# Kernel tuning notes

Measured on AMD Instinct MI355X. Metric: run time of the kernel, lower is better.

## Reference

```python
import jax, jax.numpy as jnp
import numpy as np

B, N, C, H = 4, 8192, 1024, 16
D = C // H

def setup_inputs() -> dict:
    key = jax.random.key(0)
    k1, k2, k3 = jax.random.split(key, 3)
    scale_in = 1.0 / np.sqrt(C)
    return {
        "x": jax.random.normal(k1, (B, N, C), dtype=jnp.float32),
        "w_qkv": jax.random.normal(k2, (C, 3 * C), dtype=jnp.float32) * scale_in,
        "b_qkv": jnp.zeros((3 * C,), dtype=jnp.float32),
        "w_proj": jax.random.normal(k3, (C, C), dtype=jnp.float32) * scale_in,
        "b_proj": jnp.zeros((C,), dtype=jnp.float32),
    }

def reference(x, w_qkv, b_qkv, w_proj, b_proj):
    Bx, Nx, Cx = x.shape
    qkv = x @ w_qkv + b_qkv                       # [B,N,3C]
    qkv = qkv.reshape(Bx, Nx, 3, H, D)
    qkv = jnp.transpose(qkv, (2, 0, 3, 1, 4))     # [3,B,H,N,D]
    q, k, v = qkv[0], qkv[1], qkv[2]
    q = jax.nn.elu(q) + 1.0                       # positive feature map
    k = jax.nn.elu(k) + 1.0
    kv = jnp.einsum('bhnd,bhne->bhde', k, v)      # [B,H,D,D]
    out = jnp.einsum('bhnd,bhde->bhne', q, kv)    # [B,H,N,D]
    z = 1.0 / (jnp.einsum('bhnd,bhd->bhn', q, k.sum(axis=2)) + 1e-8)
    out = out * z[..., None]
    out = jnp.transpose(out, (0, 2, 1, 3)).reshape(Bx, Nx, Cx)
    out = out @ w_proj + b_proj                   # dropout is identity in eval
    return out
```

## Files before the change

### kernel.cpp

```cpp
#include <hip/hip_runtime.h>
#include <hip/hip_bf16.h>
#include <stdint.h>

typedef unsigned short ushort_t;
typedef __attribute__((ext_vector_type(8))) short short8;
typedef __attribute__((ext_vector_type(4))) float floatx4;

__device__ __forceinline__ ushort_t f2b(float f) {
    unsigned u = __float_as_uint(f);
    unsigned r = (u + 0x7FFFu + ((u >> 16) & 1u)) >> 16;
    return (ushort_t)r;
}
__device__ __forceinline__ float b2f(ushort_t h) {
    return __uint_as_float(((unsigned)h) << 16);
}
__device__ __forceinline__ float elu1(float f) {
    return (f > 0.f) ? (f + 1.f) : __expf(f);
}

#define GLDS16(srcp, dstp)                                                          \
    __builtin_amdgcn_global_load_lds(                                               \
        (const __attribute__((address_space(1))) unsigned int*)(srcp),              \
        (__attribute__((address_space(3))) unsigned int*)(dstp), 16, 0, 0)


__global__ void conv_bf16(const float* __restrict__ in, ushort_t* __restrict__ out, int n8) {
    for (int i = blockIdx.x * blockDim.x + threadIdx.x; i < n8; i += gridDim.x * blockDim.x) {
        const float4 f0 = *(const float4*)&in[(size_t)i * 8];
        const float4 f1 = *(const float4*)&in[(size_t)i * 8 + 4];
        ushort4 o0, o1;
        o0.x = f2b(f0.x); o0.y = f2b(f0.y); o0.z = f2b(f0.z); o0.w = f2b(f0.w);
        o1.x = f2b(f1.x); o1.y = f2b(f1.y); o1.z = f2b(f1.z); o1.w = f2b(f1.w);
        *(ushort4*)&out[(size_t)i * 8]     = o0;
        *(ushort4*)&out[(size_t)i * 8 + 4] = o1;
    }
}

__global__ void transpose_conv(const float* __restrict__ in, ushort_t* __restrict__ out,
                               int R, int C) {
    __shared__ float tile[32][33];
    int c0 = blockIdx.x * 32, r0 = blockIdx.y * 32;
    int tx = threadIdx.x, ty = threadIdx.y;
#pragma unroll
    for (int k = 0; k < 4; ++k) {
        int a = ty * 4 + k;
        tile[a][tx] = in[(size_t)(r0 + a) * C + c0 + tx];
    }
    __syncthreads();
#pragma unroll
    for (int k = 0; k < 4; ++k) {
        int a = ty * 4 + k;
        out[(size_t)(c0 + a) * R + r0 + tx] = f2b(tile[tx][a]);
    }
}

__global__ void zero_f32(float* __restrict__ p, int n) {
    int i = blockIdx.x * blockDim.x + threadIdx.x;
    if (i < n) p[i] = 0.f;
}

template<int MODE>
__global__ __launch_bounds__(512, 2) void gemm256(
    const ushort_t* __restrict__ A, const ushort_t* __restrict__ Bt,
    const float* __restrict__ bias,
    ushort_t* __restrict__ out_u16, float* __restrict__ out_f32,
    int Nt, int nbx)
{
    extern __shared__ ushort_t lds[];
    constexpr int KK = 1024;

    const int tid  = threadIdx.x;
    const int wave = tid >> 6;
    const int lane = tid & 63;
    const int wm_i = wave >> 2;
    const int wn_i = wave & 3;
    const int fr   = lane & 15;
    const int fq   = lane >> 4;

    const int nwg = (int)gridDim.x;
    const int bid = (int)blockIdx.x;
    const int swz = (bid & 7) * (nwg >> 3) + (bid >> 3);
    const int bx = swz % nbx, by = swz / nbx;
    const int m0 = by * 256, n0 = bx * 256;

    const int trow = tid >> 3;
    const int csw  = ((tid & 7) ^ (trow & 7)) << 3;
    const int tcolB = ((tid >> 8) << 6) + (trow & 31);

    const ushort_t* sa = A  + (size_t)(m0 + trow)  * KK + csw;
    const ushort_t* sb = Bt + (size_t)(n0 + tcolB) * KK + csw;

    const int dstA = wave * 512;
    const int dstB = 16384 + wave * 512;

    const int sw0 = (fq ^ (fr & 7)) << 3;
    const int sw1 = sw0 ^ 32;
    const int abase = (wm_i * 64 + fr) * 64;
    const int bbase = (wn_i * 32 + fr) * 64;
    int loA0[2][2], loA1[2][2], loB0[2][2], loB1[2][2];
#pragma unroll
    for (int bf = 0; bf < 2; ++bf)
#pragma unroll
        for (int q = 0; q < 2; ++q) {
            loA0[bf][q] = bf * 32768 + q * 8192 + abase + sw0;
            loA1[bf][q] = bf * 32768 + q * 8192 + abase + sw1;
            loB0[bf][q] = bf * 32768 + 16384 + q * 8192 + bbase + sw0;
            loB1[bf][q] = bf * 32768 + 16384 + q * 8192 + bbase + sw1;
        }

    floatx4 acc[8][4];
    const floatx4 z4 = {0.f, 0.f, 0.f, 0.f};
#pragma unroll
    for (int i = 0; i < 8; ++i)
#pragma unroll
        for (int j = 0; j < 4; ++j) acc[i][j] = z4;

    short8 a[4][2], b[2][2];

    auto stageA = [&](int buf, int h, int ko) {
        ushort_t* d = lds + buf * 32768 + h * 8192 + dstA;
        GLDS16(sa + h * (64 * KK) + ko, d);
        GLDS16(sa + h * (64 * KK) + 128 * KK + ko, d + 4096);
    };
    auto stageB = [&](int buf, int h, int ko) {
        ushort_t* d = lds + buf * 32768 + h * 8192 + dstB;
        GLDS16(sb + h * (32 * KK) + ko, d);
        GLDS16(sb + h * (32 * KK) + 128 * KK + ko, d + 4096);
    };
    auto loadA = [&](int buf, int qr) {
        const int o0 = loA0[buf][qr], o1 = loA1[buf][qr];
#pragma unroll
        for (int i = 0; i < 4; ++i) {
            a[i][0] = *(const short8*)(lds + o0 + i * 1024);
            a[i][1] = *(const short8*)(lds + o1 + i * 1024);
        }
    };
    auto loadB = [&](int buf, int qc) {
        const int o0 = loB0[buf][qc], o1 = loB1[buf][qc];
#pragma unroll
        for (int j = 0; j < 2; ++j) {
            b[j][0] = *(const short8*)(lds + o0 + j * 1024);
            b[j][1] = *(const short8*)(lds + o1 + j * 1024);
        }
    };
    auto mma = [&](int qr, int qc) {
#pragma unroll
        for (int i = 0; i < 4; ++i)
#pragma unroll
            for (int j = 0; j < 2; ++j) {
                acc[qr * 4 + i][qc * 2 + j] =
                    __builtin_amdgcn_mfma_f32_16x16x32_bf16(b[j][0], a[i][0], acc[qr * 4 + i][qc * 2 + j], 0, 0, 0);
                acc[qr * 4 + i][qc * 2 + j] =
                    __builtin_amdgcn_mfma_f32_16x16x32_bf16(b[j][1], a[i][1], acc[qr * 4 + i][qc * 2 + j], 0, 0, 0);
            }
    };

#define PRIO1() __builtin_amdgcn_s_setprio(1)
#define BOUT()  __builtin_amdgcn_s_setprio(0); __builtin_amdgcn_s_barrier()
#define VM6()   asm volatile("s_waitcnt vmcnt(6)" ::: "memory")
#define VM0()   asm volatile("s_waitcnt vmcnt(0)" ::: "memory")

    stageA(0, 0, 0);
    stageB(0, 1, 0);
    stageA(0, 1, 0);
    stageB(0, 0, 0);
    stageA(1, 0, 64);
    stageB(1, 1, 64);
    stageA(1, 1, 64);
    VM6();
    __builtin_amdgcn_s_barrier();

    int ko = 0;
    for (int pr = 0; pr < 7; ++pr, ko += 128) {
        loadA(0, 0); loadB(0, 0);
        stageB(1, 0, ko + 64);
        PRIO1(); mma(0, 0); BOUT();

        loadB(0, 1);
        stageA(0, 0, ko + 128);
        PRIO1(); mma(0, 1); BOUT();

        loadA(0, 1);
        stageB(0, 1, ko + 128);
        PRIO1(); mma(1, 1); BOUT();

        loadB(0, 0);
        stageA(0, 1, ko + 128);
        PRIO1(); mma(1, 0); __builtin_amdgcn_s_setprio(0); VM6();
        __builtin_amdgcn_s_barrier();

        loadA(1, 0); loadB(1, 0);
        stageB(0, 0, ko + 128);
        PRIO1(); mma(0, 0); BOUT();

        loadB(1, 1);
        stageA(1, 0, ko + 192);
        PRIO1(); mma(0, 1); BOUT();

        loadA(1, 1);
        stageB(1, 1, ko + 192);
        PRIO1(); mma(1, 1); BOUT();

        loadB(1, 0);
        stageA(1, 1, ko + 192);
        PRIO1(); mma(1, 0); __builtin_amdgcn_s_setprio(0); VM6();
        __builtin_amdgcn_s_barrier();
    }

    loadA(0, 0); loadB(0, 0);
    stageB(1, 0, 960);
    PRIO1(); mma(0, 0); BOUT();

    loadB(0, 1);
    PRIO1(); mma(0, 1); BOUT();

    loadA(0, 1);
    PRIO1(); mma(1, 1); BOUT();

    loadB(0, 0);
    PRIO1(); mma(1, 0); __builtin_amdgcn_s_setprio(0); VM0();
    __builtin_amdgcn_s_barrier();

    loadA(1, 0); loadB(1, 0);
    PRIO1(); mma(0, 0); BOUT();

    loadB(1, 1);
    PRIO1(); mma(0, 1); BOUT();

    loadA(1, 1);
    PRIO1(); mma(1, 1); BOUT();

    loadB(1, 0);
    PRIO1(); mma(1, 0);
    __builtin_amdgcn_s_setprio(0);

#undef PRIO1
#undef BOUT
#undef VM6
#undef VM0

    float4 bv[4];
#pragma unroll
    for (int cj = 0; cj < 4; ++cj) {
        const int nb = n0 + wn_i * 64 + (cj >> 1) * 32 + (cj & 1) * 16 + fq * 4;
        bv[cj] = *(const float4*)&bias[nb];
    }
#pragma unroll
    for (int ri = 0; ri < 8; ++ri) {
        const int m = m0 + wm_i * 128 + (ri >> 2) * 64 + (ri & 3) * 16 + fr;
#pragma unroll
        for (int cj = 0; cj < 4; ++cj) {
            const int col = n0 + wn_i * 64 + (cj >> 1) * 32 + (cj & 1) * 16 + fq * 4;
            if (MODE == 0) {
                const int s = col >> 10;
                const int c = col & 1023;
                const int h = c >> 6;
                const int d = c & 63;
                const int bb = m >> 13;
                const int n  = m & 8191;
                float v0 = acc[ri][cj][0] + bv[cj].x;
                float v1 = acc[ri][cj][1] + bv[cj].y;
                float v2 = acc[ri][cj][2] + bv[cj].z;
                float v3 = acc[ri][cj][3] + bv[cj].w;
                if (s < 2) { v0 = elu1(v0); v1 = elu1(v1); v2 = elu1(v2); v3 = elu1(v3); }
                ushort4 o;
                o.x = f2b(v0); o.y = f2b(v1); o.z = f2b(v2); o.w = f2b(v3);
                *(ushort4*)&out_u16[(((size_t)s * 64 + bb * 16 + h) * 8192 + n) * 64 + d] = o;
            } else {
                float4 o;
                o.x = acc[ri][cj][0] + bv[cj].x;
                o.y = acc[ri][cj][1] + bv[cj].y;
                o.z = acc[ri][cj][2] + bv[cj].z;
                o.w = acc[ri][cj][3] + bv[cj].w;
                *(float4*)&out_f32[(size_t)m * Nt + col] = o;
            }
        }
    }
}

__global__ __launch_bounds__(256) void kv_kernel(
    const ushort_t* __restrict__ kbuf, const ushort_t* __restrict__ vbuf,
    float* __restrict__ kv, float* __restrict__ ksum)
{
    __shared__ ushort_t ks[64 * 64] __attribute__((aligned(16)));
    __shared__ ushort_t vs[64 * 64] __attribute__((aligned(16)));

    const int bh = blockIdx.y, chunk = blockIdx.x, t = threadIdx.x;
    const int d0 = (t >> 4) * 4, e0 = (t & 15) * 4;
    const bool do_ksum = (t & 15) == 0;

    float acc[4][4];
#pragma unroll
    for (int i = 0; i < 4; ++i)
#pragma unroll
        for (int j = 0; j < 4; ++j) acc[i][j] = 0.f;
    float kacc[4] = {0.f, 0.f, 0.f, 0.f};

    for (int sub = 0; sub < 8; ++sub) {
        const int nb = chunk * 512 + sub * 64;
        __syncthreads();
#pragma unroll
        for (int p = 0; p < 2; ++p) {
            int idx = p * 256 + t;
            int r = idx >> 3, c = (idx & 7) * 8;
            *(short8*)&ks[r * 64 + c] = *(const short8*)&kbuf[((size_t)bh * 8192 + nb + r) * 64 + c];
            *(short8*)&vs[r * 64 + c] = *(const short8*)&vbuf[((size_t)bh * 8192 + nb + r) * 64 + c];
        }
        __syncthreads();
        for (int n = 0; n < 64; ++n) {
            ushort4 kd = *(const ushort4*)&ks[n * 64 + d0];
            ushort4 ve = *(const ushort4*)&vs[n * 64 + e0];
            float kf[4] = {b2f(kd.x), b2f(kd.y), b2f(kd.z), b2f(kd.w)};
            float vf[4] = {b2f(ve.x), b2f(ve.y), b2f(ve.z), b2f(ve.w)};
#pragma unroll
            for (int i = 0; i < 4; ++i) {
#pragma unroll
                for (int j = 0; j < 4; ++j) acc[i][j] += kf[i] * vf[j];
            }
            if (do_ksum) {
#pragma unroll
                for (int i = 0; i < 4; ++i) kacc[i] += kf[i];
            }
        }
    }
#pragma unroll
    for (int i = 0; i < 4; ++i) {
        if (do_ksum) atomicAdd(&ksum[bh * 64 + d0 + i], kacc[i]);
#pragma unroll
        for (int j = 0; j < 4; ++j)
            atomicAdd(&kv[((size_t)bh * 64 + d0 + i) * 64 + e0 + j], acc[i][j]);
    }
}

__global__ __launch_bounds__(256) void out_kernel(
    const ushort_t* __restrict__ qbuf, const float* __restrict__ kv,
    const float* __restrict__ ksum, ushort_t* __restrict__ obuf)
{
    __shared__ float kvs[4096];
    __shared__ float ksums[64];

    const int bh = blockIdx.y, chunk = blockIdx.x, t = threadIdx.x;
    const int b = bh >> 4, h = bh & 15;
    const int wave = t >> 6, lane = t & 63;
    const int tok = lane & 15, fq = lane >> 4;

#pragma unroll
    for (int i = 0; i < 4; ++i) {
        int idx = (i * 256 + t) * 4;
        *(float4*)&kvs[idx] = *(const float4*)&kv[(size_t)bh * 4096 + idx];
    }
    if (t < 64) ksums[t] = ksum[bh * 64 + t];
    __syncthreads();

    short8 afr[4][2];
#pragma unroll
    for (int et = 0; et < 4; ++et)
#pragma unroll
        for (int kslice = 0; kslice < 2; ++kslice)
#pragma unroll
            for (int i = 0; i < 8; ++i) {
                const int d = kslice * 32 + fq * 8 + i;
                afr[et][kslice][i] = (short)f2b(kvs[d * 64 + et * 16 + tok]);
            }
    short8 zfr[2];
#pragma unroll
    for (int kslice = 0; kslice < 2; ++kslice)
#pragma unroll
        for (int i = 0; i < 8; ++i)
            zfr[kslice][i] = (short)f2b(ksums[kslice * 32 + fq * 8 + i]);

    const floatx4 z4 = {0.f, 0.f, 0.f, 0.f};
    const int nbase = chunk * 1024 + wave * 256;
    const ushort_t* qrow = qbuf + ((size_t)bh * 8192 + nbase + tok) * 64 + fq * 8;
    ushort_t* orow = obuf + ((size_t)b * 8192 + nbase + tok) * 1024 + h * 64 + fq * 4;

#pragma unroll 2
    for (int g = 0; g < 16; ++g) {
        short8 bf0 = *(const short8*)(qrow + (size_t)g * 16 * 64);
        short8 bf1 = *(const short8*)(qrow + (size_t)g * 16 * 64 + 32);

        floatx4 az = __builtin_amdgcn_mfma_f32_16x16x32_bf16(zfr[0], bf0, z4, 0, 0, 0);
        az = __builtin_amdgcn_mfma_f32_16x16x32_bf16(zfr[1], bf1, az, 0, 0, 0);

        floatx4 ad[4];
#pragma unroll
        for (int et = 0; et < 4; ++et) {
            ad[et] = __builtin_amdgcn_mfma_f32_16x16x32_bf16(afr[et][0], bf0, z4, 0, 0, 0);
            ad[et] = __builtin_amdgcn_mfma_f32_16x16x32_bf16(afr[et][1], bf1, ad[et], 0, 0, 0);
        }

        const float zi = 1.f / (az[0] + 1e-8f);
#pragma unroll
        for (int et = 0; et < 4; ++et) {
            ushort4 o;
            o.x = f2b(ad[et][0] * zi);
            o.y = f2b(ad[et][1] * zi);
            o.z = f2b(ad[et][2] * zi);
            o.w = f2b(ad[et][3] * zi);
            *(ushort4*)&orow[(size_t)g * 16 * 1024 + et * 16] = o;
        }
    }
}


extern "C" void kernel_launch(void* const* d_in, const int* in_sizes, int n_in,
                              void* d_out, int out_size, void* d_ws, size_t ws_size,
                              hipStream_t stream) {
    const float* x      = (const float*)d_in[0];
    const float* w_qkv  = (const float*)d_in[1];
    const float* b_qkv  = (const float*)d_in[2];
    const float* w_proj = (const float*)d_in[3];
    const float* b_proj = (const float*)d_in[4];
    float* out = (float*)d_out;

    const size_t XE = (size_t)32768 * 1024;

    char* ws = (char*)d_ws;
    ushort_t* xb   = (ushort_t*)ws;  ws += XE * 2;
    ushort_t* wqT  = (ushort_t*)ws;  ws += (size_t)3072 * 1024 * 2;
    ushort_t* wpT  = (ushort_t*)ws;  ws += (size_t)1024 * 1024 * 2;
    ushort_t* qkvb = (ushort_t*)ws;  ws += 3 * XE * 2;
    ushort_t* ob   = (ushort_t*)ws;  ws += XE * 2;
    float*    kv   = (float*)ws;     ws += (size_t)64 * 64 * 64 * 4;
    float*    ksum = (float*)ws;     ws += (size_t)64 * 64 * 4;

    (void)hipFuncSetAttribute(reinterpret_cast<const void*>(gemm256<0>),
                              hipFuncAttributeMaxDynamicSharedMemorySize, 131072);
    (void)hipFuncSetAttribute(reinterpret_cast<const void*>(gemm256<1>),
                              hipFuncAttributeMaxDynamicSharedMemorySize, 131072);

    zero_f32<<<dim3((64 * 64 * 64 + 64 * 64 + 255) / 256), dim3(256), 0, stream>>>(kv, 64 * 64 * 64 + 64 * 64);
    conv_bf16<<<dim3(2048), dim3(256), 0, stream>>>(x, xb, (int)(XE / 8));
    transpose_conv<<<dim3(96, 32), dim3(32, 8), 0, stream>>>(w_qkv, wqT, 1024, 3072);
    transpose_conv<<<dim3(32, 32), dim3(32, 8), 0, stream>>>(w_proj, wpT, 1024, 1024);

    gemm256<0><<<dim3(1536), dim3(512), 131072, stream>>>(xb, wqT, b_qkv, qkvb, nullptr, 3072, 12);

    kv_kernel<<<dim3(16, 64), dim3(256), 0, stream>>>(qkvb + XE, qkvb + 2 * XE, kv, ksum);
    out_kernel<<<dim3(8, 64), dim3(256), 0, stream>>>(qkvb, kv, ksum, ob);

    gemm256<1><<<dim3(512), dim3(512), 131072, stream>>>(ob, wpT, b_proj, nullptr, out, 1024, 4);
}
```

Baseline: 490.3 us.

## Switch GEMM inner product to 32x32x16 bf16 MFMA tiles

Replaces the 16x16x32 MFMA fragments in the 256x256 GEMM with 32x32x16 MFMA instructions. This changes the LDS read fragment layout, the accumulator shape (floatx16), and the epilogue index mapping. The larger MFMA issues fewer instructions and gets more reuse per LDS read, at the cost of a different swizzle access pattern that may cause LDS bank conflicts. The epilogue also uses the hardware packed bf16 convert instruction instead of manual rounding.

```diff
diff --git a/kernel.cpp b/kernel.cpp
--- a/kernel.cpp
+++ b/kernel.cpp
@@ -5,6 +5,7 @@
 typedef unsigned short ushort_t;
 typedef __attribute__((ext_vector_type(8))) short short8;
 typedef __attribute__((ext_vector_type(4))) float floatx4;
+typedef __attribute__((ext_vector_type(16))) float floatx16;
 
 __device__ __forceinline__ ushort_t f2b(float f) {
     unsigned u = __float_as_uint(f);
@@ -16,6 +17,11 @@
 }
 __device__ __forceinline__ float elu1(float f) {
     return (f > 0.f) ? (f + 1.f) : __expf(f);
+}
+__device__ __forceinline__ unsigned cvtpk(float lo, float hi) {
+    unsigned w;
+    asm("v_cvt_pk_bf16_f32 %0, %1, %2" : "=v"(w) : "v"(lo), "v"(hi));
+    return w;
 }
 
 #define GLDS16(srcp, dstp)                                                          \
@@ -74,8 +80,8 @@
     const int lane = tid & 63;
     const int wm_i = wave >> 2;
     const int wn_i = wave & 3;
-    const int fr   = lane & 15;
-    const int fq   = lane >> 4;
+    const int ml   = lane & 31;
+    const int fh   = lane >> 5;
 
     const int nwg = (int)gridDim.x;
     const int bid = (int)blockIdx.x;
@@ -93,29 +99,21 @@
     const int dstA = wave * 512;
     const int dstB = 16384 + wave * 512;
 
-    const int sw0 = (fq ^ (fr & 7)) << 3;
-    const int sw1 = sw0 ^ 32;
-    const int abase = (wm_i * 64 + fr) * 64;
-    const int bbase = (wn_i * 32 + fr) * 64;
-    int loA0[2][2], loA1[2][2], loB0[2][2], loB1[2][2];
-#pragma unroll
-    for (int bf = 0; bf < 2; ++bf)
-#pragma unroll
-        for (int q = 0; q < 2; ++q) {
-            loA0[bf][q] = bf * 32768 + q * 8192 + abase + sw0;
-            loA1[bf][q] = bf * 32768 + q * 8192 + abase + sw1;
-            loB0[bf][q] = bf * 32768 + 16384 + q * 8192 + bbase + sw0;
-            loB1[bf][q] = bf * 32768 + 16384 + q * 8192 + bbase + sw1;
-        }
-
-    floatx4 acc[8][4];
-    const floatx4 z4 = {0.f, 0.f, 0.f, 0.f};
-#pragma unroll
-    for (int i = 0; i < 8; ++i)
-#pragma unroll
-        for (int j = 0; j < 4; ++j) acc[i][j] = z4;
-
-    short8 a[4][2], b[2][2];
+    int pcs[4];
+#pragma unroll
+    for (int s = 0; s < 4; ++s) pcs[s] = (((s * 2 + fh) ^ (lane & 7)) << 3);
+    const int rbA = (wm_i * 64 + ml) << 6;
+    const int rbB = (wn_i * 32 + ml) << 6;
+
+    floatx16 acc[4][2];
+#pragma unroll
+    for (int i = 0; i < 4; ++i)
+#pragma unroll
+        for (int j = 0; j < 2; ++j)
+#pragma unroll
+            for (int e = 0; e < 16; ++e) acc[i][j][e] = 0.f;
+
+    short8 a32[2][4], b32[4];
 
     auto stageA = [&](int buf, int h, int ko) {
         ushort_t* d = lds + buf * 32768 + h * 8192 + dstA;
@@ -128,31 +126,27 @@
         GLDS16(sb + h * (32 * KK) + 128 * KK + ko, d + 4096);
     };
     auto loadA = [&](int buf, int qr) {
-        const int o0 = loA0[buf][qr], o1 = loA1[buf][qr];
-#pragma unroll
-        for (int i = 0; i < 4; ++i) {
-            a[i][0] = *(const short8*)(lds + o0 + i * 1024);
-            a[i][1] = *(const short8*)(lds + o1 + i * 1024);
-        }
+        const int base = buf * 32768 + qr * 8192 + rbA;
+#pragma unroll
+        for (int i = 0; i < 2; ++i)
+#pragma unroll
+            for (int s = 0; s < 4; ++s)
+                a32[i][s] = *(const short8*)(lds + base + i * 2048 + pcs[s]);
     };
     auto loadB = [&](int buf, int qc) {
-        const int o0 = loB0[buf][qc], o1 = loB1[buf][qc];
-#pragma unroll
-        for (int j = 0; j < 2; ++j) {
-            b[j][0] = *(const short8*)(lds + o0 + j * 1024);
-            b[j][1] = *(const short8*)(lds + o1 + j * 1024);
-        }
+        const int base = buf * 32768 + 16384 + qc * 8192 + rbB;
+#pragma unroll
+        for (int s = 0; s < 4; ++s)
+            b32[s] = *(const short8*)(lds + base + pcs[s]);
     };
     auto mma = [&](int qr, int qc) {
 #pragma unroll
-        for (int i = 0; i < 4; ++i)
-#pragma unroll
-            for (int j = 0; j < 2; ++j) {
-                acc[qr * 4 + i][qc * 2 + j] =
-                    __builtin_amdgcn_mfma_f32_16x16x32_bf16(b[j][0], a[i][0], acc[qr * 4 + i][qc * 2 + j], 0, 0, 0);
-                acc[qr * 4 + i][qc * 2 + j] =
-                    __builtin_amdgcn_mfma_f32_16x16x32_bf16(b[j][1], a[i][1], acc[qr * 4 + i][qc * 2 + j], 0, 0, 0);
-            }
+        for (int s = 0; s < 4; ++s) {
+            acc[qr * 2 + 0][qc] =
+                __builtin_amdgcn_mfma_f32_32x32x16_bf16(b32[s], a32[0][s], acc[qr * 2 + 0][qc], 0, 0, 0);
+            acc[qr * 2 + 1][qc] =
+                __builtin_amdgcn_mfma_f32_32x32x16_bf16(b32[s], a32[1][s], acc[qr * 2 + 1][qc], 0, 0, 0);
+        }
     };
 
 #define PRIO1() __builtin_amdgcn_s_setprio(1)
@@ -239,40 +233,42 @@
 #undef VM6
 #undef VM0
 
-    float4 bv[4];
-#pragma unroll
-    for (int cj = 0; cj < 4; ++cj) {
-        const int nb = n0 + wn_i * 64 + (cj >> 1) * 32 + (cj & 1) * 16 + fq * 4;
-        bv[cj] = *(const float4*)&bias[nb];
-    }
-#pragma unroll
-    for (int ri = 0; ri < 8; ++ri) {
-        const int m = m0 + wm_i * 128 + (ri >> 2) * 64 + (ri & 3) * 16 + fr;
-#pragma unroll
-        for (int cj = 0; cj < 4; ++cj) {
-            const int col = n0 + wn_i * 64 + (cj >> 1) * 32 + (cj & 1) * 16 + fq * 4;
-            if (MODE == 0) {
-                const int s = col >> 10;
-                const int c = col & 1023;
-                const int h = c >> 6;
-                const int d = c & 63;
-                const int bb = m >> 13;
-                const int n  = m & 8191;
-                float v0 = acc[ri][cj][0] + bv[cj].x;
-                float v1 = acc[ri][cj][1] + bv[cj].y;
-                float v2 = acc[ri][cj][2] + bv[cj].z;
-                float v3 = acc[ri][cj][3] + bv[cj].w;
-                if (s < 2) { v0 = elu1(v0); v1 = elu1(v1); v2 = elu1(v2); v3 = elu1(v3); }
-                ushort4 o;
-                o.x = f2b(v0); o.y = f2b(v1); o.z = f2b(v2); o.w = f2b(v3);
-                *(ushort4*)&out_u16[(((size_t)s * 64 + bb * 16 + h) * 8192 + n) * 64 + d] = o;
-            } else {
-                float4 o;
-                o.x = acc[ri][cj][0] + bv[cj].x;
-                o.y = acc[ri][cj][1] + bv[cj].y;
-                o.z = acc[ri][cj][2] + bv[cj].z;
-                o.w = acc[ri][cj][3] + bv[cj].w;
-                *(float4*)&out_f32[(size_t)m * Nt + col] = o;
+    float4 bvv[2][4];
+#pragma unroll
+    for (int qch = 0; qch < 2; ++qch)
+#pragma unroll
+        for (int g = 0; g < 4; ++g) {
+            const int nb = n0 + wn_i * 64 + qch * 32 + 8 * g + 4 * fh;
+            bvv[qch][g] = *(const float4*)&bias[nb];
+        }
+#pragma unroll
+    for (int mt = 0; mt < 4; ++mt) {
+        const int m = m0 + wm_i * 128 + mt * 32 + ml;
+#pragma unroll
+        for (int qch = 0; qch < 2; ++qch) {
+#pragma unroll
+            for (int g = 0; g < 4; ++g) {
+                const int nb = n0 + wn_i * 64 + qch * 32 + 8 * g + 4 * fh;
+                float v0 = acc[mt][qch][4 * g + 0] + bvv[qch][g].x;
+                float v1 = acc[mt][qch][4 * g + 1] + bvv[qch][g].y;
+                float v2 = acc[mt][qch][4 * g + 2] + bvv[qch][g].z;
+                float v3 = acc[mt][qch][4 * g + 3] + bvv[qch][g].w;
+                if (MODE == 0) {
+                    const int s  = nb >> 10;
+                    const int c  = nb & 1023;
+                    const int hh = c >> 6;
+                    const int d  = c & 63;
+                    const int bb = m >> 13;
+                    const int nt = m & 8191;
+                    if (s < 2) { v0 = elu1(v0); v1 = elu1(v1); v2 = elu1(v2); v3 = elu1(v3); }
+                    uint2 o;
+                    o.x = cvtpk(v0, v1);
+                    o.y = cvtpk(v2, v3);
+                    *(uint2*)&out_u16[(((size_t)s * 64 + bb * 16 + hh) * 8192 + nt) * 64 + d] = o;
+                } else {
+                    float4 o; o.x = v0; o.y = v1; o.z = v2; o.w = v3;
+                    *(float4*)&out_f32[(size_t)m * Nt + nb] = o;
+                }
             }
         }
     }
```

Result: slower. 534.8 us (+9.1%).

## Compute K^T V with MFMA using transposed K/V layout from QKV GEMM epilogue

Applied to the files above, without the earlier changes.

The QKV GEMM epilogue now writes K and V transposed (d-major, token-contiguous), so a new kernel can load token strips per head-dim row and run bf16 MFMA to form K^T V, with ksum obtained by an MFMA against a ones vector. Per-wave partials are reduced in LDS before the atomics, and the grid uses fewer, larger chunks. This replaces the scalar FMA outer-product loop, which was ALU bound. The cost is that the epilogue's K/V writes become scattered 2-byte stores with a large stride instead of vectorized ushort4 stores, which may slow the GEMM.

```diff
diff --git a/kernel.cpp b/kernel.cpp
--- a/kernel.cpp
+++ b/kernel.cpp
@@ -68,6 +68,7 @@
 {
     extern __shared__ ushort_t lds[];
     constexpr int KK = 1024;
+    constexpr size_t XEc = (size_t)32768 * 1024;
 
     const int tid  = threadIdx.x;
     const int wave = tid >> 6;
@@ -251,84 +252,146 @@
 #pragma unroll
         for (int cj = 0; cj < 4; ++cj) {
             const int col = n0 + wn_i * 64 + (cj >> 1) * 32 + (cj & 1) * 16 + fq * 4;
+            float v0 = acc[ri][cj][0] + bv[cj].x;
+            float v1 = acc[ri][cj][1] + bv[cj].y;
+            float v2 = acc[ri][cj][2] + bv[cj].z;
+            float v3 = acc[ri][cj][3] + bv[cj].w;
             if (MODE == 0) {
-                const int s = col >> 10;
-                const int c = col & 1023;
-                const int h = c >> 6;
-                const int d = c & 63;
+                const int s  = col >> 10;
+                const int c  = col & 1023;
+                const int h  = c >> 6;
+                const int d  = c & 63;
                 const int bb = m >> 13;
                 const int n  = m & 8191;
-                float v0 = acc[ri][cj][0] + bv[cj].x;
-                float v1 = acc[ri][cj][1] + bv[cj].y;
-                float v2 = acc[ri][cj][2] + bv[cj].z;
-                float v3 = acc[ri][cj][3] + bv[cj].w;
-                if (s < 2) { v0 = elu1(v0); v1 = elu1(v1); v2 = elu1(v2); v3 = elu1(v3); }
-                ushort4 o;
-                o.x = f2b(v0); o.y = f2b(v1); o.z = f2b(v2); o.w = f2b(v3);
-                *(ushort4*)&out_u16[(((size_t)s * 64 + bb * 16 + h) * 8192 + n) * 64 + d] = o;
+                const int bh = bb * 16 + h;
+                if (s == 0) {
+                    v0 = elu1(v0); v1 = elu1(v1); v2 = elu1(v2); v3 = elu1(v3);
+                    ushort4 o;
+                    o.x = f2b(v0); o.y = f2b(v1); o.z = f2b(v2); o.w = f2b(v3);
+                    *(ushort4*)&out_u16[((size_t)bh * 8192 + n) * 64 + d] = o;
+                } else if (s == 1) {
+                    v0 = elu1(v0); v1 = elu1(v1); v2 = elu1(v2); v3 = elu1(v3);
+                    ushort_t* kT = out_u16 + XEc;
+                    kT[((size_t)bh * 64 + d + 0) * 8192 + n] = f2b(v0);
+                    kT[((size_t)bh * 64 + d + 1) * 8192 + n] = f2b(v1);
+                    kT[((size_t)bh * 64 + d + 2) * 8192 + n] = f2b(v2);
+                    kT[((size_t)bh * 64 + d + 3) * 8192 + n] = f2b(v3);
+                } else {
+                    ushort_t* vT = out_u16 + 2 * XEc;
+                    vT[((size_t)bh * 64 + d + 0) * 8192 + n] = f2b(v0);
+                    vT[((size_t)bh * 64 + d + 1) * 8192 + n] = f2b(v1);
+                    vT[((size_t)bh * 64 + d + 2) * 8192 + n] = f2b(v2);
+                    vT[((size_t)bh * 64 + d + 3) * 8192 + n] = f2b(v3);
+                }
             } else {
-                float4 o;
-                o.x = acc[ri][cj][0] + bv[cj].x;
-                o.y = acc[ri][cj][1] + bv[cj].y;
-                o.z = acc[ri][cj][2] + bv[cj].z;
-                o.w = acc[ri][cj][3] + bv[cj].w;
+                float4 o; o.x = v0; o.y = v1; o.z = v2; o.w = v3;
                 *(float4*)&out_f32[(size_t)m * Nt + col] = o;
             }
         }
     }
 }
 
-__global__ __launch_bounds__(256) void kv_kernel(
-    const ushort_t* __restrict__ kbuf, const ushort_t* __restrict__ vbuf,
+__global__ __launch_bounds__(256) void kvg_kernel(
+    const ushort_t* __restrict__ kT, const ushort_t* __restrict__ vT,
     float* __restrict__ kv, float* __restrict__ ksum)
 {
-    __shared__ ushort_t ks[64 * 64] __attribute__((aligned(16)));
-    __shared__ ushort_t vs[64 * 64] __attribute__((aligned(16)));
+    __shared__ ushort_t stg[4][2][4096] __attribute__((aligned(16)));
+    __shared__ float ksr[4][64];
 
     const int bh = blockIdx.y, chunk = blockIdx.x, t = threadIdx.x;
-    const int d0 = (t >> 4) * 4, e0 = (t & 15) * 4;
-    const bool do_ksum = (t & 15) == 0;
-
-    float acc[4][4];
-#pragma unroll
-    for (int i = 0; i < 4; ++i)
-#pragma unroll
-        for (int j = 0; j < 4; ++j) acc[i][j] = 0.f;
-    float kacc[4] = {0.f, 0.f, 0.f, 0.f};
-
-    for (int sub = 0; sub < 8; ++sub) {
-        const int nb = chunk * 512 + sub * 64;
-        __syncthreads();
-#pragma unroll
-        for (int p = 0; p < 2; ++p) {
-            int idx = p * 256 + t;
-            int r = idx >> 3, c = (idx & 7) * 8;
-            *(short8*)&ks[r * 64 + c] = *(const short8*)&kbuf[((size_t)bh * 8192 + nb + r) * 64 + c];
-            *(short8*)&vs[r * 64 + c] = *(const short8*)&vbuf[((size_t)bh * 8192 + nb + r) * 64 + c];
-        }
-        __syncthreads();
-        for (int n = 0; n < 64; ++n) {
-            ushort4 kd = *(const ushort4*)&ks[n * 64 + d0];
-            ushort4 ve = *(const ushort4*)&vs[n * 64 + e0];
-            float kf[4] = {b2f(kd.x), b2f(kd.y), b2f(kd.z), b2f(kd.w)};
-            float vf[4] = {b2f(ve.x), b2f(ve.y), b2f(ve.z), b2f(ve.w)};
-#pragma unroll
-            for (int i = 0; i < 4; ++i) {
-#pragma unroll
-                for (int j = 0; j < 4; ++j) acc[i][j] += kf[i] * vf[j];
+    const int wave = t >> 6, lane = t & 63;
+    const int tok = lane & 15, fq = lane >> 4;
+
+    int roff[4][2];
+#pragma unroll
+    for (int rt = 0; rt < 4; ++rt) {
+        const int row = rt * 16 + tok;
+        const int S = (row & 7) ^ (((row >> 3) & 3) << 1);
+#pragma unroll
+        for (int s = 0; s < 2; ++s)
+            roff[rt][s] = row * 64 + (((4 * s + fq) ^ S) << 3);
+    }
+    const int Sw = (lane & 7) ^ (((lane >> 3) & 3) << 1);
+
+    short8 ones;
+#pragma unroll
+    for (int i = 0; i < 8; ++i) ones[i] = (short)0x3F80;
+
+    floatx4 av[4][4], ak[4];
+    const floatx4 z4 = {0.f, 0.f, 0.f, 0.f};
+#pragma unroll
+    for (int i = 0; i < 4; ++i) {
+        ak[i] = z4;
+#pragma unroll
+        for (int j = 0; j < 4; ++j) av[i][j] = z4;
+    }
+
+    const ushort_t* srcK = kT + ((size_t)bh * 64 + lane) * 8192 + chunk * 1024;
+    const ushort_t* srcV = vT + ((size_t)bh * 64 + lane) * 8192 + chunk * 1024;
+    ushort_t* dk = &stg[wave][0][lane * 64];
+    ushort_t* dv = &stg[wave][1][lane * 64];
+
+#pragma unroll 1
+    for (int s2 = 0; s2 < 4; ++s2) {
+        const int ns = (wave * 4 + s2) * 64;
+#pragma unroll
+        for (int g = 0; g < 8; ++g) {
+            const int ph = (g ^ Sw) << 3;
+            *(short8*)&dk[ph] = *(const short8*)&srcK[ns + g * 8];
+            *(short8*)&dv[ph] = *(const short8*)&srcV[ns + g * 8];
+        }
+#pragma unroll
+        for (int s = 0; s < 2; ++s) {
+            short8 afr[4], bfr[4];
+#pragma unroll
+            for (int rt = 0; rt < 4; ++rt)
+                afr[rt] = *(const short8*)&stg[wave][0][roff[rt][s]];
+#pragma unroll
+            for (int rt = 0; rt < 4; ++rt)
+                bfr[rt] = *(const short8*)&stg[wave][1][roff[rt][s]];
+#pragma unroll
+            for (int dt = 0; dt < 4; ++dt) {
+                ak[dt] = __builtin_amdgcn_mfma_f32_16x16x32_bf16(afr[dt], ones, ak[dt], 0, 0, 0);
+#pragma unroll
+                for (int et = 0; et < 4; ++et)
+                    av[dt][et] = __builtin_amdgcn_mfma_f32_16x16x32_bf16(afr[dt], bfr[et], av[dt][et], 0, 0, 0);
             }
-            if (do_ksum) {
-#pragma unroll
-                for (int i = 0; i < 4; ++i) kacc[i] += kf[i];
-            }
-        }
-    }
-#pragma unroll
-    for (int i = 0; i < 4; ++i) {
-        if (do_ksum) atomicAdd(&ksum[bh * 64 + d0 + i], kacc[i]);
-#pragma unroll
-        for (int j = 0; j < 4; ++j)
-            atomicAdd(&kv[((size_t)bh * 64 + d0 + i) * 64 + e0 + j], acc[i][j]);
+        }
+    }
+
+    float* red = (float*)&stg[wave][0][0];
+#pragma unroll
+    for (int dt = 0; dt < 4; ++dt)
+#pragma unroll
+        for (int et = 0; et < 4; ++et)
+#pragma unroll
+            for (int r = 0; r < 4; ++r)
+                red[(dt * 16 + fq * 4 + r) * 64 + et * 16 + tok] = av[dt][et][r];
+    if (tok == 0) {
+#pragma unroll
+        for (int dt = 0; dt < 4; ++dt)
+#pragma unroll
+            for (int r = 0; r < 4; ++r)
+                ksr[wave][dt * 16 + fq * 4 + r] = ak[dt][r];
+    }
+    __syncthreads();
+
+    const float* base = (const float*)&stg[0][0][0];
+#pragma unroll
+    for (int j = 0; j < 4; ++j) {
+        const int idx = t * 16 + j * 4;
+        float4 s0 = *(const float4*)&base[0 * 4096 + idx];
+        float4 s1 = *(const float4*)&base[1 * 4096 + idx];
+        float4 s2 = *(const float4*)&base[2 * 4096 + idx];
+        float4 s3 = *(const float4*)&base[3 * 4096 + idx];
+        atomicAdd(&kv[(size_t)bh * 4096 + idx + 0], s0.x + s1.x + s2.x + s3.x);
+        atomicAdd(&kv[(size_t)bh * 4096 + idx + 1], s0.y + s1.y + s2.y + s3.y);
+        atomicAdd(&kv[(size_t)bh * 4096 + idx + 2], s0.z + s1.z + s2.z + s3.z);
+        atomicAdd(&kv[(size_t)bh * 4096 + idx + 3], s0.w + s1.w + s2.w + s3.w);
+    }
+    if (t < 64) {
+        float s = ksr[0][t] + ksr[1][t] + ksr[2][t] + ksr[3][t];
+        atomicAdd(&ksum[bh * 64 + t], s);
     }
 }
 
@@ -436,7 +499,7 @@
 
     gemm256<0><<<dim3(1536), dim3(512), 131072, stream>>>(xb, wqT, b_qkv, qkvb, nullptr, 3072, 12);
 
-    kv_kernel<<<dim3(16, 64), dim3(256), 0, stream>>>(qkvb + XE, qkvb + 2 * XE, kv, ksum);
+    kvg_kernel<<<dim3(8, 64), dim3(256), 0, stream>>>(qkvb + XE, qkvb + 2 * XE, kv, ksum);
     out_kernel<<<dim3(8, 64), dim3(256), 0, stream>>>(qkvb, kv, ksum, ob);
 
     gemm256<1><<<dim3(512), dim3(512), 131072, stream>>>(ob, wpT, b_proj, nullptr, out, 1024, 4);
```

New measurement: 507.5 us. +3.5%, slower.

## Make GEMM persistent with cross-tile prefetch of next tile's operands

Applied to the files above, without the earlier changes.

Converts the 256x256 GEMM kernel into a persistent kernel launched with 256 workgroups, each looping over several output tiles strided by 256. The final K-steps of each tile now stage the first two K-slices of the next tile, so loading the next tile's operands overlaps the current tile's tail compute and epilogue. This removes per-tile launch, ramp-up and drain bubbles. In exchange it fixes the grid at 256 workgroups, which can leave compute units idle or unevenly loaded, and it replaces the previous bid-based swizzle with a simpler tile ordering that may hurt L2 reuse.

```diff
diff --git a/kernel.cpp b/kernel.cpp
--- a/kernel.cpp
+++ b/kernel.cpp
@@ -64,7 +64,7 @@
     const ushort_t* __restrict__ A, const ushort_t* __restrict__ Bt,
     const float* __restrict__ bias,
     ushort_t* __restrict__ out_u16, float* __restrict__ out_f32,
-    int Nt, int nbx)
+    int Nt, int nbx, int nt)
 {
     extern __shared__ ushort_t lds[];
     constexpr int KK = 1024;
@@ -77,18 +77,13 @@
     const int fr   = lane & 15;
     const int fq   = lane >> 4;
 
-    const int nwg = (int)gridDim.x;
-    const int bid = (int)blockIdx.x;
-    const int swz = (bid & 7) * (nwg >> 3) + (bid >> 3);
-    const int bx = swz % nbx, by = swz / nbx;
-    const int m0 = by * 256, n0 = bx * 256;
+    const int bid  = (int)blockIdx.x;
+    const int bswz = ((bid & 7) << 5) + (bid >> 3);
+    const int ntiles = nt << 8;
 
     const int trow = tid >> 3;
     const int csw  = ((tid & 7) ^ (trow & 7)) << 3;
     const int tcolB = ((tid >> 8) << 6) + (trow & 31);
-
-    const ushort_t* sa = A  + (size_t)(m0 + trow)  * KK + csw;
-    const ushort_t* sb = Bt + (size_t)(n0 + tcolB) * KK + csw;
 
     const int dstA = wave * 512;
     const int dstB = 16384 + wave * 512;
@@ -117,15 +112,23 @@
 
     short8 a[4][2], b[2][2];
 
-    auto stageA = [&](int buf, int h, int ko) {
+    auto tilebase = [&](int t, const ushort_t*& sA, const ushort_t*& sB, int& mm, int& nn) {
+        const int byy = t / nbx;
+        const int bxx = t - byy * nbx;
+        mm = byy << 8; nn = bxx << 8;
+        sA = A  + (size_t)(mm + trow)  * KK + csw;
+        sB = Bt + (size_t)(nn + tcolB) * KK + csw;
+    };
+
+    auto stageA = [&](const ushort_t* sp, int buf, int h, int ko) {
         ushort_t* d = lds + buf * 32768 + h * 8192 + dstA;
-        GLDS16(sa + h * (64 * KK) + ko, d);
-        GLDS16(sa + h * (64 * KK) + 128 * KK + ko, d + 4096);
-    };
-    auto stageB = [&](int buf, int h, int ko) {
+        GLDS16(sp + h * (64 * KK) + ko, d);
+        GLDS16(sp + h * (64 * KK) + 128 * KK + ko, d + 4096);
+    };
+    auto stageB = [&](const ushort_t* sp, int buf, int h, int ko) {
         ushort_t* d = lds + buf * 32768 + h * 8192 + dstB;
-        GLDS16(sb + h * (32 * KK) + ko, d);
-        GLDS16(sb + h * (32 * KK) + 128 * KK + ko, d + 4096);
+        GLDS16(sp + h * (32 * KK) + ko, d);
+        GLDS16(sp + h * (32 * KK) + 128 * KK + ko, d + 4096);
     };
     auto loadA = [&](int buf, int qr) {
         const int o0 = loA0[buf][qr], o1 = loA1[buf][qr];
@@ -155,127 +158,149 @@
             }
     };
 
-#define PRIO1() __builtin_amdgcn_s_setprio(1)
-#define BOUT()  __builtin_amdgcn_s_setprio(0); __builtin_amdgcn_s_barrier()
-#define VM6()   asm volatile("s_waitcnt vmcnt(6)" ::: "memory")
-#define VM0()   asm volatile("s_waitcnt vmcnt(0)" ::: "memory")
-
-    stageA(0, 0, 0);
-    stageB(0, 1, 0);
-    stageA(0, 1, 0);
-    stageB(0, 0, 0);
-    stageA(1, 0, 64);
-    stageB(1, 1, 64);
-    stageA(1, 1, 64);
-    VM6();
-    __builtin_amdgcn_s_barrier();
-
-    int ko = 0;
-    for (int pr = 0; pr < 7; ++pr, ko += 128) {
-        loadA(0, 0); loadB(0, 0);
-        stageB(1, 0, ko + 64);
-        PRIO1(); mma(0, 0); BOUT();
-
-        loadB(0, 1);
-        stageA(0, 0, ko + 128);
-        PRIO1(); mma(0, 1); BOUT();
-
-        loadA(0, 1);
-        stageB(0, 1, ko + 128);
-        PRIO1(); mma(1, 1); BOUT();
-
-        loadB(0, 0);
-        stageA(0, 1, ko + 128);
-        PRIO1(); mma(1, 0); __builtin_amdgcn_s_setprio(0); VM6();
-        __builtin_amdgcn_s_barrier();
-
-        loadA(1, 0); loadB(1, 0);
-        stageB(0, 0, ko + 128);
-        PRIO1(); mma(0, 0); BOUT();
-
-        loadB(1, 1);
-        stageA(1, 0, ko + 192);
-        PRIO1(); mma(0, 1); BOUT();
-
-        loadA(1, 1);
-        stageB(1, 1, ko + 192);
-        PRIO1(); mma(1, 1); BOUT();
-
-        loadB(1, 0);
-        stageA(1, 1, ko + 192);
-        PRIO1(); mma(1, 0); __builtin_amdgcn_s_setprio(0); VM6();
-        __builtin_amdgcn_s_barrier();
-    }
-
-    loadA(0, 0); loadB(0, 0);
-    stageB(1, 0, 960);
-    PRIO1(); mma(0, 0); BOUT();
-
-    loadB(0, 1);
-    PRIO1(); mma(0, 1); BOUT();
-
-    loadA(0, 1);
-    PRIO1(); mma(1, 1); BOUT();
-
-    loadB(0, 0);
-    PRIO1(); mma(1, 0); __builtin_amdgcn_s_setprio(0); VM0();
-    __builtin_amdgcn_s_barrier();
-
-    loadA(1, 0); loadB(1, 0);
-    PRIO1(); mma(0, 0); BOUT();
-
-    loadB(1, 1);
-    PRIO1(); mma(0, 1); BOUT();
-
-    loadA(1, 1);
-    PRIO1(); mma(1, 1); BOUT();
-
-    loadB(1, 0);
-    PRIO1(); mma(1, 0);
-    __builtin_amdgcn_s_setprio(0);
-
-#undef PRIO1
-#undef BOUT
-#undef VM6
-#undef VM0
-
-    float4 bv[4];
-#pragma unroll
-    for (int cj = 0; cj < 4; ++cj) {
-        const int nb = n0 + wn_i * 64 + (cj >> 1) * 32 + (cj & 1) * 16 + fq * 4;
-        bv[cj] = *(const float4*)&bias[nb];
-    }
-#pragma unroll
-    for (int ri = 0; ri < 8; ++ri) {
-        const int m = m0 + wm_i * 128 + (ri >> 2) * 64 + (ri & 3) * 16 + fr;
+    auto epilogue = [&](int m0, int n0) {
+        float4 bv[4];
 #pragma unroll
         for (int cj = 0; cj < 4; ++cj) {
-            const int col = n0 + wn_i * 64 + (cj >> 1) * 32 + (cj & 1) * 16 + fq * 4;
-            if (MODE == 0) {
-                const int s = col >> 10;
-                const int c = col & 1023;
-                const int h = c >> 6;
-                const int d = c & 63;
-                const int bb = m >> 13;
-                const int n  = m & 8191;
+            const int nb = n0 + wn_i * 64 + (cj >> 1) * 32 + (cj & 1) * 16 + fq * 4;
+            bv[cj] = *(const float4*)&bias[nb];
+        }
+#pragma unroll
+        for (int ri = 0; ri < 8; ++ri) {
+            const int m = m0 + wm_i * 128 + (ri >> 2) * 64 + (ri & 3) * 16 + fr;
+#pragma unroll
+            for (int cj = 0; cj < 4; ++cj) {
+                const int col = n0 + wn_i * 64 + (cj >> 1) * 32 + (cj & 1) * 16 + fq * 4;
                 float v0 = acc[ri][cj][0] + bv[cj].x;
                 float v1 = acc[ri][cj][1] + bv[cj].y;
                 float v2 = acc[ri][cj][2] + bv[cj].z;
                 float v3 = acc[ri][cj][3] + bv[cj].w;
-                if (s < 2) { v0 = elu1(v0); v1 = elu1(v1); v2 = elu1(v2); v3 = elu1(v3); }
-                ushort4 o;
-                o.x = f2b(v0); o.y = f2b(v1); o.z = f2b(v2); o.w = f2b(v3);
-                *(ushort4*)&out_u16[(((size_t)s * 64 + bb * 16 + h) * 8192 + n) * 64 + d] = o;
-            } else {
-                float4 o;
-                o.x = acc[ri][cj][0] + bv[cj].x;
-                o.y = acc[ri][cj][1] + bv[cj].y;
-                o.z = acc[ri][cj][2] + bv[cj].z;
-                o.w = acc[ri][cj][3] + bv[cj].w;
-                *(float4*)&out_f32[(size_t)m * Nt + col] = o;
+                if (MODE == 0) {
+                    const int s  = col >> 10;
+                    const int c  = col & 1023;
+                    const int h  = c >> 6;
+                    const int d  = c & 63;
+                    const int bb = m >> 13;
+                    const int n  = m & 8191;
+                    if (s < 2) { v0 = elu1(v0); v1 = elu1(v1); v2 = elu1(v2); v3 = elu1(v3); }
+                    ushort4 o;
+                    o.x = f2b(v0); o.y = f2b(v1); o.z = f2b(v2); o.w = f2b(v3);
+                    *(ushort4*)&out_u16[(((size_t)s * 64 + bb * 16 + h) * 8192 + n) * 64 + d] = o;
+                } else {
+                    float4 o; o.x = v0; o.y = v1; o.z = v2; o.w = v3;
+                    *(float4*)&out_f32[(size_t)m * Nt + col] = o;
+                }
             }
         }
-    }
+    };
+
+#define PRIO1() __builtin_amdgcn_s_setprio(1)
+#define BOUT()  __builtin_amdgcn_s_setprio(0); __builtin_amdgcn_s_barrier()
+#define VM6()   asm volatile("s_waitcnt vmcnt(6)" ::: "memory")
+
+    const ushort_t *saC, *sbC, *saN, *sbN;
+    int m0, n0, m0N, n0N;
+    int tC = bswz;
+    tilebase(tC, saC, sbC, m0, n0);
+    int tN = (tC + 256 < ntiles) ? tC + 256 : tC;
+    tilebase(tN, saN, sbN, m0N, n0N);
+
+    stageA(saC, 0, 0, 0);
+    stageB(sbC, 0, 1, 0);
+    stageA(saC, 0, 1, 0);
+    stageB(sbC, 0, 0, 0);
+    stageA(saC, 1, 0, 64);
+    stageB(sbC, 1, 1, 64);
+    stageA(saC, 1, 1, 64);
+    VM6();
+    __builtin_amdgcn_s_barrier();
+
+    for (int ot = 0; ot < nt; ++ot) {
+        int ko = 0;
+        for (int pr = 0; pr < 7; ++pr, ko += 128) {
+            loadA(0, 0); loadB(0, 0);
+            stageB(sbC, 1, 0, ko + 64);
+            PRIO1(); mma(0, 0); BOUT();
+
+            loadB(0, 1);
+            stageA(saC, 0, 0, ko + 128);
+            PRIO1(); mma(0, 1); BOUT();
+
+            loadA(0, 1);
+            stageB(sbC, 0, 1, ko + 128);
+            PRIO1(); mma(1, 1); BOUT();
+
+            loadB(0, 0);
+            stageA(saC, 0, 1, ko + 128);
+            PRIO1(); mma(1, 0); __builtin_amdgcn_s_setprio(0); VM6();
+            __builtin_amdgcn_s_barrier();
+
+            loadA(1, 0); loadB(1, 0);
+            stageB(sbC, 0, 0, ko + 128);
+            PRIO1(); mma(0, 0); BOUT();
+
+            loadB(1, 1);
+            stageA(saC, 1, 0, ko + 192);
+            PRIO1(); mma(0, 1); BOUT();
+
+            loadA(1, 1);
+            stageB(sbC, 1, 1, ko + 192);
+            PRIO1(); mma(1, 1); BOUT();
+
+            loadB(1, 0);
+            stageA(saC, 1, 1, ko + 192);
+            PRIO1(); mma(1, 0); __builtin_amdgcn_s_setprio(0); VM6();
+            __builtin_amdgcn_s_barrier();
+        }
+
+        loadA(0, 0); loadB(0, 0);
+        stageB(sbC, 1, 0, 960);
+        PRIO1(); mma(0, 0); BOUT();
+
+        loadB(0, 1);
+        stageA(saN, 0, 0, 0);
+        PRIO1(); mma(0, 1); BOUT();
+
+        loadA(0, 1);
+        stageB(sbN, 0, 1, 0);
+        PRIO1(); mma(1, 1); BOUT();
+
+        loadB(0, 0);
+        stageA(saN, 0, 1, 0);
+        PRIO1(); mma(1, 0); __builtin_amdgcn_s_setprio(0); VM6();
+        __builtin_amdgcn_s_barrier();
+
+        loadA(1, 0); loadB(1, 0);
+        stageB(sbN, 0, 0, 0);
+        PRIO1(); mma(0, 0); BOUT();
+
+        loadB(1, 1);
+        stageA(saN, 1, 0, 64);
+        PRIO1(); mma(0, 1); BOUT();
+
+        loadA(1, 1);
+        stageB(sbN, 1, 1, 64);
+        PRIO1(); mma(1, 1); BOUT();
+
+        loadB(1, 0);
+        stageA(saN, 1, 1, 64);
+        PRIO1(); mma(1, 0); __builtin_amdgcn_s_setprio(0); VM6();
+        __builtin_amdgcn_s_barrier();
+
+        epilogue(m0, n0);
+#pragma unroll
+        for (int i = 0; i < 8; ++i)
+#pragma unroll
+            for (int j = 0; j < 4; ++j) acc[i][j] = z4;
+
+        saC = saN; sbC = sbN; m0 = m0N; n0 = n0N; tC = tN;
+        tN = (tC + 256 < ntiles) ? tC + 256 : tC;
+        tilebase(tN, saN, sbN, m0N, n0N);
+    }
+
+#undef PRIO1
+#undef BOUT
+#undef VM6
 }
 
 __global__ __launch_bounds__(256) void kv_kernel(
@@ -434,10 +459,10 @@
     transpose_conv<<<dim3(96, 32), dim3(32, 8), 0, stream>>>(w_qkv, wqT, 1024, 3072);
     transpose_conv<<<dim3(32, 32), dim3(32, 8), 0, stream>>>(w_proj, wpT, 1024, 1024);
 
-    gemm256<0><<<dim3(1536), dim3(512), 131072, stream>>>(xb, wqT, b_qkv, qkvb, nullptr, 3072, 12);
+    gemm256<0><<<dim3(256), dim3(512), 131072, stream>>>(xb, wqT, b_qkv, qkvb, nullptr, 3072, 12, 6);
 
     kv_kernel<<<dim3(16, 64), dim3(256), 0, stream>>>(qkvb + XE, qkvb + 2 * XE, kv, ksum);
     out_kernel<<<dim3(8, 64), dim3(256), 0, stream>>>(qkvb, kv, ksum, ob);
 
-    gemm256<1><<<dim3(512), dim3(512), 131072, stream>>>(ob, wpT, b_proj, nullptr, out, 1024, 4);
-}
+    gemm256<1><<<dim3(256), dim3(512), 131072, stream>>>(ob, wpT, b_proj, nullptr, out, 1024, 4, 2);
+}
```

Measured after the change: 475.2 us. 3.1% less time.
